# Optimization experiments

Measured on AMD Instinct MI355X. Metric: run time of the kernel, lower is better.

Reference implementation:

```python
import jax, jax.numpy as jnp
import numpy as np

K = 3
STRIDE = 1
PAD = 1


def _unfold(x, k, stride, pad):
    # x: (B, C, H, W) -> (B, C*k*k, L) matching torch.nn.functional.unfold
    # ordering: channel slowest, then kh, then kw.
    B, C, H, W = x.shape
    Hout = (H + 2 * pad - k) // stride + 1
    Wout = (W + 2 * pad - k) // stride + 1
    xp = jnp.pad(x, ((0, 0), (0, 0), (pad, pad), (pad, pad)))
    patches = []  # fixed k*k loop (9 iters), not a data-dim loop
    for i in range(k):
        for j in range(k):
            patches.append(xp[:, :, i:i + stride * Hout:stride, j:j + stride * Wout:stride])
    # (B, C, k*k, Hout, Wout) -> (B, C*k*k, L)
    p = jnp.stack(patches, axis=2)
    return p.reshape(B, C * k * k, Hout * Wout), Hout, Wout


def setup_inputs() -> dict:
    key = jax.random.key(0)
    k1, k2 = jax.random.split(key)
    x = jax.random.normal(k1, (4, 32, 56, 56), dtype=jnp.float32)
    weights = jax.random.normal(k2, (64, 32, 3, 3), dtype=jnp.float32)
    return {"x": x, "weights": weights}


def reference(x, weights):
    B = x.shape[0]
    O = weights.shape[0]
    mu_w = jnp.mean(jnp.abs(weights))
    x_unf, Hout, Wout = _unfold(x, K, STRIDE, PAD)      # (B, Ckk, L)
    w_unf = weights.reshape(O, -1)                        # (O, Ckk)
    # min-plus 'convolution': broadcast min then reduce over patch dim
    min_val = jnp.minimum(x_unf[:, None, :, :], w_unf[None, :, :, None])  # (B, O, Ckk, L)
    z = mu_w * jnp.sum(min_val, axis=2)                   # (B, O, L)
    return z.reshape(B, O, Hout, Wout)
```

## Files before the change

### kernel.cpp

```cpp
#include <hip/hip_runtime.h>

#define CIN  32
#define OCH  64
#define HH   56
#define WW   56
#define BB   4
#define OT   4
#define IMG  (HH * WW)
#define NW   18432
#define PH   58
#define PW   58
#define PIMG (PH * PW)
#define NXPK (BB * (CIN/2) * PIMG)
#define XPKBLKS (NXPK / 256)
#define NWPK (OCH * (CIN/2) * 9)
#define WPKBLKS (NWPK / 256)
#define WOFFu 64
#define XOFFu (WOFFu + NWPK)

typedef _Float16 h2 __attribute__((ext_vector_type(2)));

static __device__ __forceinline__ h2 pkmin_vv(h2 xv, unsigned wu) {
    unsigned xu = __builtin_bit_cast(unsigned, xv);
    unsigned ru;
    asm("v_pk_min_f16 %0, %1, %2" : "=v"(ru) : "v"(xu), "v"(wu));
    return __builtin_bit_cast(h2, ru);
}

__global__ __launch_bounds__(256) void prep(const float* __restrict__ x,
                                            const float* __restrict__ w,
                                            float* __restrict__ ws) {
    unsigned* wsu = reinterpret_cast<unsigned*>(ws);
    if (blockIdx.x < XPKBLKS) {
        int idx = blockIdx.x * 256 + threadIdx.x;
        int bc  = idx / PIMG;
        int r   = idx - bc * PIMG;
        int ph  = r / PW;
        int pw  = r - ph * PW;
        int hh  = ph - 1, wc = pw - 1;
        float v0 = 0.f, v1 = 0.f;
        if ((unsigned)hh < (unsigned)HH && (unsigned)wc < (unsigned)WW) {
            int base = ((bc >> 4) * CIN + (bc & 15) * 2) * IMG + hh * WW + wc;
            v0 = x[base];
            v1 = x[base + IMG];
        }
        h2 p; p.x = (_Float16)v0; p.y = (_Float16)v1;
        wsu[XOFFu + idx] = __builtin_bit_cast(unsigned, p);
        return;
    }
    if (blockIdx.x < XPKBLKS + WPKBLKS) {
        int idx = (blockIdx.x - XPKBLKS) * 256 + threadIdx.x;
        int otile = idx / 576;
        int r     = idx - otile * 576;
        int wv4   = r / 144;
        int r2    = r - wv4 * 144;
        int cl    = r2 / 36;
        int r3    = r2 - cl * 36;
        int t     = r3 >> 2;
        int oo    = r3 & 3;
        int o     = otile * OT + oo;
        int cp    = wv4 * 4 + cl;
        int src   = o * (CIN * 9) + cp * 18 + t;
        h2 p; p.x = (_Float16)w[src]; p.y = (_Float16)w[src + 9];
        wsu[WOFFu + idx] = __builtin_bit_cast(unsigned, p);
        return;
    }
    float s = 0.f;
    const float4* w4 = reinterpret_cast<const float4*>(w);
    #pragma unroll
    for (int k = 0; k < 18; ++k) {
        float4 v = w4[k * 256 + threadIdx.x];
        s += fabsf(v.x) + fabsf(v.y) + fabsf(v.z) + fabsf(v.w);
    }
    #pragma unroll
    for (int off = 32; off; off >>= 1) s += __shfl_down(s, off);
    __shared__ float sm[4];
    if ((threadIdx.x & 63) == 0) sm[threadIdx.x >> 6] = s;
    __syncthreads();
    if (threadIdx.x == 0)
        ws[0] = (sm[0] + sm[1] + sm[2] + sm[3]) * (1.0f / (float)NW);
}

__global__ __launch_bounds__(256) void minconv_kernel(const float* __restrict__ ws,
                                                      const float* __restrict__ wts,
                                                      float* __restrict__ out) {
    const unsigned* wsu = reinterpret_cast<const unsigned*>(ws);
    const int tid  = threadIdx.x;
    const int lane = tid & 63;
    const int wv   = tid >> 6;
    const int wvs  = __builtin_amdgcn_readfirstlane(wv);
    const int hw = blockIdx.x * 64 + lane;
    const int o0 = blockIdx.y * OT;
    const int b  = blockIdx.z;
    const int h  = hw / WW;
    const int w  = hw - h * WW;

    const float mu = ws[0];

    __shared__ __align__(16) unsigned wlds[576];
    __shared__ float red[4][4][64];

    {
        const unsigned* wt = wsu + WOFFu + blockIdx.y * 576;
        *reinterpret_cast<uint2*>(&wlds[tid * 2]) =
            *reinterpret_cast<const uint2*>(&wt[tid * 2]);
        if (tid < 64) wlds[512 + tid] = wt[512 + tid];
    }

    const int cp0 = wvs * 4;
    const unsigned* xq = wsu + XOFFu + (size_t)(b * 16 + cp0) * PIMG + h * PW + w;

    __syncthreads();

    h2 ones; ones.x = (_Float16)1.f; ones.y = (_Float16)1.f;
    float a0 = 0.f, a1 = 0.f, a2 = 0.f, a3 = 0.f;
    const unsigned* wl = wlds + wv * 144;

    #pragma unroll
    for (int cl = 0; cl < 4; ++cl) {
        h2 xv[9];
        #pragma unroll
        for (int kh = 0; kh < 3; ++kh)
            #pragma unroll
            for (int kw = 0; kw < 3; ++kw)
                xv[kh * 3 + kw] =
                    __builtin_bit_cast(h2, xq[cl * PIMG + kh * PW + kw]);
        #pragma unroll
        for (int t = 0; t < 9; ++t) {
            uint4 q = *reinterpret_cast<const uint4*>(&wl[cl * 36 + t * 4]);
            h2 m0 = pkmin_vv(xv[t], q.x);
            a0 = __builtin_amdgcn_fdot2(m0, ones, a0, false);
            h2 m1 = pkmin_vv(xv[t], q.y);
            a1 = __builtin_amdgcn_fdot2(m1, ones, a1, false);
            h2 m2 = pkmin_vv(xv[t], q.z);
            a2 = __builtin_amdgcn_fdot2(m2, ones, a2, false);
            h2 m3 = pkmin_vv(xv[t], q.w);
            a3 = __builtin_amdgcn_fdot2(m3, ones, a3, false);
        }
    }

    red[wv][0][lane] = a0;
    red[wv][1][lane] = a1;
    red[wv][2][lane] = a2;
    red[wv][3][lane] = a3;
    __syncthreads();

    float s = red[0][wv][lane] + red[1][wv][lane]
            + red[2][wv][lane] + red[3][wv][lane];
    out[((size_t)b * OCH + o0 + wv) * IMG + hw] = mu * s;
}

extern "C" void kernel_launch(void* const* d_in, const int* in_sizes, int n_in,
                              void* d_out, int out_size, void* d_ws, size_t ws_size,
                              hipStream_t stream) {
    const float* x   = (const float*)d_in[0];
    const float* w   = (const float*)d_in[1];
    float*       out = (float*)d_out;
    float*       ws  = (float*)d_ws;

    prep<<<XPKBLKS + WPKBLKS + 1, 256, 0, stream>>>(x, w, ws);
    dim3 grid(IMG / 64, OCH / OT, BB);
    minconv_kernel<<<grid, 256, 0, stream>>>(ws, w, out);
}
```

Measured before the change: 67.79 us.

## Pack eight input channels per pixel as uint4 for wide loads in min-conv

```diff
diff --git a/kernel.cpp b/kernel.cpp
--- a/kernel.cpp
+++ b/kernel.cpp
@@ -11,8 +11,8 @@
 #define PH   58
 #define PW   58
 #define PIMG (PH * PW)
-#define NXPK (BB * (CIN/2) * PIMG)
-#define XPKBLKS (NXPK / 256)
+#define XP4  (BB * 4 * PIMG)
+#define XP4BLKS ((XP4 + 255) / 256)
 #define NWPK (OCH * (CIN/2) * 9)
 #define WPKBLKS (NWPK / 256)
 #define WOFFu 64
@@ -26,40 +26,51 @@
     asm("v_pk_min_f16 %0, %1, %2" : "=v"(ru) : "v"(xu), "v"(wu));
     return __builtin_bit_cast(h2, ru);
 }
+static __device__ __forceinline__ h2 ld_h2(unsigned u) {
+    return __builtin_bit_cast(h2, u);
+}
 
 __global__ __launch_bounds__(256) void prep(const float* __restrict__ x,
                                             const float* __restrict__ w,
                                             float* __restrict__ ws) {
     unsigned* wsu = reinterpret_cast<unsigned*>(ws);
-    if (blockIdx.x < XPKBLKS) {
+    if (blockIdx.x < XP4BLKS) {
         int idx = blockIdx.x * 256 + threadIdx.x;
-        int bc  = idx / PIMG;
-        int r   = idx - bc * PIMG;
-        int ph  = r / PW;
-        int pw  = r - ph * PW;
-        int hh  = ph - 1, wc = pw - 1;
-        float v0 = 0.f, v1 = 0.f;
-        if ((unsigned)hh < (unsigned)HH && (unsigned)wc < (unsigned)WW) {
-            int base = ((bc >> 4) * CIN + (bc & 15) * 2) * IMG + hh * WW + wc;
-            v0 = x[base];
-            v1 = x[base + IMG];
+        if (idx < XP4) {
+            int boct = idx / PIMG;
+            int pix  = idx - boct * PIMG;
+            int ph   = pix / PW;
+            int pw   = pix - ph * PW;
+            int hh   = ph - 1, wc = pw - 1;
+            int b    = boct >> 2, oct = boct & 3;
+            uint4 val = make_uint4(0u, 0u, 0u, 0u);
+            if ((unsigned)hh < (unsigned)HH && (unsigned)wc < (unsigned)WW) {
+                int src = (b * CIN + oct * 8) * IMG + hh * WW + wc;
+                unsigned* vp = &val.x;
+                #pragma unroll
+                for (int q = 0; q < 4; ++q) {
+                    h2 p;
+                    p.x = (_Float16)x[src + (2 * q) * IMG];
+                    p.y = (_Float16)x[src + (2 * q + 1) * IMG];
+                    vp[q] = __builtin_bit_cast(unsigned, p);
+                }
+            }
+            reinterpret_cast<uint4*>(wsu + XOFFu)[idx] = val;
         }
-        h2 p; p.x = (_Float16)v0; p.y = (_Float16)v1;
-        wsu[XOFFu + idx] = __builtin_bit_cast(unsigned, p);
         return;
     }
-    if (blockIdx.x < XPKBLKS + WPKBLKS) {
-        int idx = (blockIdx.x - XPKBLKS) * 256 + threadIdx.x;
+    if (blockIdx.x < XP4BLKS + WPKBLKS) {
+        int idx = (blockIdx.x - XP4BLKS) * 256 + threadIdx.x;
         int otile = idx / 576;
         int r     = idx - otile * 576;
-        int wv4   = r / 144;
-        int r2    = r - wv4 * 144;
-        int cl    = r2 / 36;
-        int r3    = r2 - cl * 36;
-        int t     = r3 >> 2;
+        int oct   = r / 144;
+        int r2    = r - oct * 144;
+        int t     = r2 / 16;
+        int r3    = r2 - t * 16;
+        int q     = r3 >> 2;
         int oo    = r3 & 3;
         int o     = otile * OT + oo;
-        int cp    = wv4 * 4 + cl;
+        int cp    = oct * 4 + q;
         int src   = o * (CIN * 9) + cp * 18 + t;
         h2 p; p.x = (_Float16)w[src]; p.y = (_Float16)w[src + 9];
         wsu[WOFFu + idx] = __builtin_bit_cast(unsigned, p);
@@ -107,42 +118,51 @@
         if (tid < 64) wlds[512 + tid] = wt[512 + tid];
     }
 
-    const int cp0 = wvs * 4;
-    const unsigned* xq = wsu + XOFFu + (size_t)(b * 16 + cp0) * PIMG + h * PW + w;
+    const uint4* xq4 = reinterpret_cast<const uint4*>(wsu + XOFFu)
+                     + (size_t)(b * 4 + wvs) * PIMG + h * PW + w;
 
     __syncthreads();
 
     h2 ones; ones.x = (_Float16)1.f; ones.y = (_Float16)1.f;
-    float a0 = 0.f, a1 = 0.f, a2 = 0.f, a3 = 0.f;
+    float a0e = 0.f, a1e = 0.f, a2e = 0.f, a3e = 0.f;
+    float a0o = 0.f, a1o = 0.f, a2o = 0.f, a3o = 0.f;
     const unsigned* wl = wlds + wv * 144;
 
     #pragma unroll
-    for (int cl = 0; cl < 4; ++cl) {
-        h2 xv[9];
+    for (int kh = 0; kh < 3; ++kh) {
         #pragma unroll
-        for (int kh = 0; kh < 3; ++kh)
-            #pragma unroll
-            for (int kw = 0; kw < 3; ++kw)
-                xv[kh * 3 + kw] =
-                    __builtin_bit_cast(h2, xq[cl * PIMG + kh * PW + kw]);
-        #pragma unroll
-        for (int t = 0; t < 9; ++t) {
-            uint4 q = *reinterpret_cast<const uint4*>(&wl[cl * 36 + t * 4]);
-            h2 m0 = pkmin_vv(xv[t], q.x);
-            a0 = __builtin_amdgcn_fdot2(m0, ones, a0, false);
-            h2 m1 = pkmin_vv(xv[t], q.y);
-            a1 = __builtin_amdgcn_fdot2(m1, ones, a1, false);
-            h2 m2 = pkmin_vv(xv[t], q.z);
-            a2 = __builtin_amdgcn_fdot2(m2, ones, a2, false);
-            h2 m3 = pkmin_vv(xv[t], q.w);
-            a3 = __builtin_amdgcn_fdot2(m3, ones, a3, false);
+        for (int kw = 0; kw < 3; ++kw) {
+            const int t = kh * 3 + kw;
+            uint4 xt = xq4[kh * PW + kw];
+            h2 x0 = ld_h2(xt.x), x1 = ld_h2(xt.y);
+            h2 x2 = ld_h2(xt.z), x3 = ld_h2(xt.w);
+            uint4 w0 = *reinterpret_cast<const uint4*>(&wl[t * 16 + 0]);
+            uint4 w1 = *reinterpret_cast<const uint4*>(&wl[t * 16 + 4]);
+            uint4 w2 = *reinterpret_cast<const uint4*>(&wl[t * 16 + 8]);
+            uint4 w3 = *reinterpret_cast<const uint4*>(&wl[t * 16 + 12]);
+            a0e = __builtin_amdgcn_fdot2(pkmin_vv(x0, w0.x), ones, a0e, false);
+            a1e = __builtin_amdgcn_fdot2(pkmin_vv(x0, w0.y), ones, a1e, false);
+            a2e = __builtin_amdgcn_fdot2(pkmin_vv(x0, w0.z), ones, a2e, false);
+            a3e = __builtin_amdgcn_fdot2(pkmin_vv(x0, w0.w), ones, a3e, false);
+            a0o = __builtin_amdgcn_fdot2(pkmin_vv(x1, w1.x), ones, a0o, false);
+            a1o = __builtin_amdgcn_fdot2(pkmin_vv(x1, w1.y), ones, a1o, false);
+            a2o = __builtin_amdgcn_fdot2(pkmin_vv(x1, w1.z), ones, a2o, false);
+            a3o = __builtin_amdgcn_fdot2(pkmin_vv(x1, w1.w), ones, a3o, false);
+            a0e = __builtin_amdgcn_fdot2(pkmin_vv(x2, w2.x), ones, a0e, false);
+            a1e = __builtin_amdgcn_fdot2(pkmin_vv(x2, w2.y), ones, a1e, false);
+            a2e = __builtin_amdgcn_fdot2(pkmin_vv(x2, w2.z), ones, a2e, false);
+            a3e = __builtin_amdgcn_fdot2(pkmin_vv(x2, w2.w), ones, a3e, false);
+            a0o = __builtin_amdgcn_fdot2(pkmin_vv(x3, w3.x), ones, a0o, false);
+            a1o = __builtin_amdgcn_fdot2(pkmin_vv(x3, w3.y), ones, a1o, false);
+            a2o = __builtin_amdgcn_fdot2(pkmin_vv(x3, w3.z), ones, a2o, false);
+            a3o = __builtin_amdgcn_fdot2(pkmin_vv(x3, w3.w), ones, a3o, false);
         }
     }
 
-    red[wv][0][lane] = a0;
-    red[wv][1][lane] = a1;
-    red[wv][2][lane] = a2;
-    red[wv][3][lane] = a3;
+    red[wv][0][lane] = a0e + a0o;
+    red[wv][1][lane] = a1e + a1o;
+    red[wv][2][lane] = a2e + a2o;
+    red[wv][3][lane] = a3e + a3o;
     __syncthreads();
 
     float s = red[0][wv][lane] + red[1][wv][lane]
@@ -158,7 +178,7 @@
     float*       out = (float*)d_out;
     float*       ws  = (float*)d_ws;
 
-    prep<<<XPKBLKS + WPKBLKS + 1, 256, 0, stream>>>(x, w, ws);
+    prep<<<XP4BLKS + WPKBLKS + 1, 256, 0, stream>>>(x, w, ws);
     dim3 grid(IMG / 64, OCH / OT, BB);
     minconv_kernel<<<grid, 256, 0, stream>>>(ws, w, out);
 }
```

Result: no change. 67.13 us (-1.0%).
